# Optimization experiments

Measured on AMD Instinct MI355X. Metric: run time of the kernel, lower is better.

The kernel has to match this reference:

```python
import jax, jax.numpy as jnp
import numpy as np

N_NODES = 50000; N_EDGES = 600000; N_GRAPHS = 128
IN_CH = 128; PROJ = 128; OUT_CH = 128; K = 3; NCLASS = 2; EPS = 1e-5


def _mask():
    # xhi_layer_mask: block i (rows i*OUT_CH:(i+1)*OUT_CH) sees first PROJ*(i+1) input cols
    blocks = []
    for i in range(K):
        m = np.zeros((OUT_CH, PROJ * K), np.float32)
        m[:, :PROJ * (i + 1)] = 1.0
        blocks.append(m)
    return jnp.asarray(np.concatenate(blocks, 0))


def _bn(x, g, b):
    # BatchNorm1d in training mode: biased batch stats, affine g/b
    m = jnp.mean(x, axis=0)
    v = jnp.var(x, axis=0)
    return (x - m) * jax.lax.rsqrt(v + EPS) * g + b


def setup_inputs() -> dict:
    key = jax.random.key(0)
    ks = jax.random.split(key, 10)
    M = OUT_CH * K
    def w(k, shape):
        return jax.random.normal(k, shape, jnp.float32) * 0.05
    return {
        "x": jax.random.normal(ks[0], (N_NODES, IN_CH), jnp.float32),
        "edge_index": jax.random.randint(ks[1], (2, N_EDGES), 0, N_NODES),
        "batch": jnp.sort(jax.random.randint(ks[2], (N_NODES,), 0, N_GRAPHS)),
        "n_graphs": N_GRAPHS,
        "w_rel": w(ks[3], (PROJ, IN_CH)), "b_rel": jnp.zeros((PROJ,), jnp.float32),
        "w_root": w(ks[4], (PROJ, IN_CH)),
        "norm0_g": jnp.ones((PROJ,), jnp.float32), "norm0_b": jnp.zeros((PROJ,), jnp.float32),
        "lin_w": w(ks[5], (M, PROJ * K)), "lin_b": jnp.zeros((M,), jnp.float32),
        "bnh_g": jnp.ones((M,), jnp.float32), "bnh_b": jnp.zeros((M,), jnp.float32),
        "bno_g": jnp.ones((3 * M,), jnp.float32), "bno_b": jnp.zeros((3 * M,), jnp.float32),
        "w1": w(ks[6], (2 * M, 3 * M)), "b1": jnp.zeros((2 * M,), jnp.float32),
        "w2": w(ks[7], (M, 2 * M)), "b2": jnp.zeros((M,), jnp.float32),
        "w3": w(ks[8], (NCLASS, M)), "b3": jnp.zeros((NCLASS,), jnp.float32),
    }


def reference(x, edge_index, batch, n_graphs, w_rel, b_rel, w_root, norm0_g, norm0_b,
              lin_w, lin_b, bnh_g, bnh_b, bno_g, bno_b, w1, b1, w2, b2, w3, b3):
    row, col = edge_index[0], edge_index[1]
    # GraphConv: lin_rel(sum_{j->i} x_j) + lin_root(x_i)
    neigh = jax.ops.segment_sum(x[row], col, num_segments=N_NODES)
    X = neigh @ w_rel.T + b_rel + x @ w_root.T
    X = _bn(X, norm0_g, norm0_b)
    # k-hop polynomial diffusion: A^i X computed as iterative SpMM over edges
    # (A[r,c] = 1 for edge (r,c): (A v)[r] = sum over edges of v[c])
    H = [X]
    cur = X
    for _ in range(K - 1):
        cur = jax.ops.segment_sum(cur[col], row, num_segments=N_NODES)
        H.append(cur)
    Hc = jnp.concatenate(H, axis=1)  # [N, PROJ*K]
    Hm = _bn(Hc @ (lin_w * _mask()).T + lin_b, bnh_g, bnh_b)  # [N, OUT_CH*K]
    # global mean / add / max pooling per graph
    ones = jnp.ones((N_NODES,), jnp.float32)
    cnt = jax.ops.segment_sum(ones, batch, num_segments=n_graphs)
    Hadd = jax.ops.segment_sum(Hm, batch, num_segments=n_graphs)
    Havg = Hadd / jnp.maximum(cnt, 1.0)[:, None]
    Hmax = jax.ops.segment_max(Hm, batch, num_segments=n_graphs)
    Hmax = jnp.where(jnp.isfinite(Hmax), Hmax, 0.0)  # guard empty segments
    Hcat = jnp.concatenate([Havg, Hadd, Hmax], axis=1)  # [G, 3*OUT_CH*K]
    # funnel readout (dropout = identity in eval)
    h = _bn(Hcat, bno_g, bno_b)
    h = jax.nn.relu(h @ w1.T + b1)
    h = jax.nn.relu(h @ w2.T + b2)
    return jax.nn.log_softmax(h @ w3.T + b3, axis=1)
```

## Files before the change

kernel.cpp:

```cpp
#include <hip/hip_runtime.h>
#include <math.h>

#define N_NODES 50000
#define N_EDGES 600000
#define N_GRAPHS 128
#define IN_CH 128
#define PROJ 128
#define OUT_CH 128
#define M_DIM 384
#define HC_DIM 384
#define CAT_DIM 1152
#define H1_DIM 768
#define EPS 1e-5f
#define SCAN_BLK 256

using bf16x8 = __attribute__((ext_vector_type(8))) short;
using f32x4  = __attribute__((ext_vector_type(4))) float;

__device__ inline unsigned short f2bf(float f) {
  unsigned u = __float_as_uint(f);
  unsigned r = u + 0x7fffu + ((u >> 16) & 1u);
  return (unsigned short)(r >> 16);
}
__device__ inline float bf2f(unsigned short h) {
  return __uint_as_float(((unsigned)h) << 16);
}

__device__ inline void atomicMaxF(float* addr, float val) {
  int iv = __float_as_int(val);
  if (iv >= 0) atomicMax((int*)addr, iv);
  else         atomicMin((unsigned int*)addr, (unsigned int)iv);
}
__device__ inline void atomicMinF(float* addr, float val) {
  int iv = __float_as_int(val);
  if (iv >= 0) atomicMin((int*)addr, iv);
  else         atomicMax((unsigned int*)addr, (unsigned int)iv);
}

__global__ void fill_minmax_kernel(float* __restrict__ gmax, float* __restrict__ gmin) {
  int i = blockIdx.x * blockDim.x + threadIdx.x;
  if (i < N_GRAPHS * M_DIM) {
    gmax[i] = -__builtin_inff();
    gmin[i] =  __builtin_inff();
  }
}

__global__ void bounds_kernel(const int* __restrict__ batch, int* __restrict__ start) {
  int i = blockIdx.x * blockDim.x + threadIdx.x;
  if (i >= N_NODES) return;
  int b = batch[i];
  int bp = (i == 0) ? -1 : batch[i - 1];
  for (int g = bp + 1; g <= b; ++g) start[g] = i;
  if (i == N_NODES - 1)
    for (int g = b + 1; g <= N_GRAPHS; ++g) start[g] = N_NODES;
}

__global__ void cnt_from_bounds_kernel(const int* __restrict__ start, float* __restrict__ cnt) {
  int g = threadIdx.x;
  if (g < N_GRAPHS) cnt[g] = (float)(start[g + 1] - start[g]);
}

__global__ void hist_kernel(const int* __restrict__ row, const int* __restrict__ col,
                            int* __restrict__ degA, int* __restrict__ degB) {
  int e = blockIdx.x * blockDim.x + threadIdx.x;
  if (e < N_EDGES) {
    atomicAdd(&degA[col[e]], 1);
    atomicAdd(&degB[row[e]], 1);
  }
}

__global__ void scan1_kernel(const int* __restrict__ deg, int* __restrict__ offs,
                             int* __restrict__ bsum, int n) {
  __shared__ int sh[SCAN_BLK];
  int i = blockIdx.x * SCAN_BLK + threadIdx.x;
  int v = (i < n) ? deg[i] : 0;
  sh[threadIdx.x] = v; __syncthreads();
  #pragma unroll
  for (int d = 1; d < SCAN_BLK; d <<= 1) {
    int t = (threadIdx.x >= d) ? sh[threadIdx.x - d] : 0;
    __syncthreads();
    sh[threadIdx.x] += t;
    __syncthreads();
  }
  if (i < n) offs[i] = sh[threadIdx.x] - v;
  if (threadIdx.x == SCAN_BLK - 1) bsum[blockIdx.x] = sh[threadIdx.x];
}

__global__ void scan2_kernel(int* __restrict__ bsum, int nb) {
  __shared__ int sh[SCAN_BLK];
  int v = (threadIdx.x < nb) ? bsum[threadIdx.x] : 0;
  sh[threadIdx.x] = v; __syncthreads();
  #pragma unroll
  for (int d = 1; d < SCAN_BLK; d <<= 1) {
    int t = (threadIdx.x >= d) ? sh[threadIdx.x - d] : 0;
    __syncthreads();
    sh[threadIdx.x] += t;
    __syncthreads();
  }
  if (threadIdx.x < nb) bsum[threadIdx.x] = sh[threadIdx.x] - v;
}

__global__ void scan3_kernel(int* __restrict__ offs, const int* __restrict__ bsum,
                             int* __restrict__ cursor, int n) {
  int i = blockIdx.x * SCAN_BLK + threadIdx.x;
  if (i < n) {
    int o = offs[i] + bsum[blockIdx.x];
    offs[i] = o;
    cursor[i] = o;
  }
}

__global__ void fill_csr_kernel(const int* __restrict__ row, const int* __restrict__ col,
                                int* __restrict__ cursA, int* __restrict__ eidxA,
                                int* __restrict__ cursB, int* __restrict__ eidxB) {
  int e = blockIdx.x * blockDim.x + threadIdx.x;
  if (e < N_EDGES) {
    int r = row[e], c = col[e];
    eidxA[atomicAdd(&cursA[c], 1)] = r;
    eidxB[atomicAdd(&cursB[r], 1)] = c;
  }
}

__global__ void convert_x_kernel(const float* __restrict__ x, unsigned short* __restrict__ xnb) {
  int t = blockIdx.x * blockDim.x + threadIdx.x;
  if (t >= N_NODES * 32) return;
  int node = t >> 5;
  int c4 = (t & 31) << 2;
  float4 v = *(const float4*)(x + (size_t)node * IN_CH + c4);
  ushort4 h = {f2bf(v.x), f2bf(v.y), f2bf(v.z), f2bf(v.w)};
  *(ushort4*)(xnb + (size_t)node * 256 + 128 + c4) = h;
}

__global__ void convert_wcat_kernel(const float* __restrict__ w_rel, const float* __restrict__ w_root,
                                    unsigned short* __restrict__ wcatb) {
  int t = blockIdx.x * blockDim.x + threadIdx.x;
  if (t >= 128 * 64) return;
  int n = t >> 6;
  int c4 = (t & 63) << 2;
  const float* src = (c4 < 128) ? (w_rel + (size_t)n * 128 + c4)
                                : (w_root + (size_t)n * 128 + (c4 - 128));
  float4 v = *(const float4*)src;
  ushort4 h = {f2bf(v.x), f2bf(v.y), f2bf(v.z), f2bf(v.w)};
  *(ushort4*)(wcatb + (size_t)n * 256 + c4) = h;
}

__global__ void convert_linw_kernel(const float* __restrict__ lin_w, unsigned short* __restrict__ linwb) {
  int t = blockIdx.x * blockDim.x + threadIdx.x;
  if (t >= 384 * 96) return;
  int n = t / 96;
  int c4 = (t - n * 96) << 2;
  float4 v = *(const float4*)(lin_w + (size_t)n * HC_DIM + c4);
  ushort4 h = {f2bf(v.x), f2bf(v.y), f2bf(v.z), f2bf(v.w)};
  *(ushort4*)(linwb + (size_t)n * HC_DIM + c4) = h;
}

__global__ __launch_bounds__(256) void gather_bf16_kernel(
    const unsigned short* __restrict__ src, const int* __restrict__ offs,
    const int* __restrict__ ends, const int* __restrict__ eidx,
    unsigned short* __restrict__ dst, int src_ld, int dst_ld) {
  int tid = blockIdx.x * blockDim.x + threadIdx.x;
  int node = tid >> 5;
  int c = (tid & 31) << 2;
  if (node >= N_NODES) return;
  int j = offs[node], end = ends[node];
  float ax = 0.f, ay = 0.f, az = 0.f, aw = 0.f;
  for (; j + 1 < end; j += 2) {
    int s0 = eidx[j], s1 = eidx[j + 1];
    ushort4 v0 = *(const ushort4*)(src + (size_t)s0 * src_ld + c);
    ushort4 v1 = *(const ushort4*)(src + (size_t)s1 * src_ld + c);
    ax += bf2f(v0.x); ay += bf2f(v0.y); az += bf2f(v0.z); aw += bf2f(v0.w);
    ax += bf2f(v1.x); ay += bf2f(v1.y); az += bf2f(v1.z); aw += bf2f(v1.w);
  }
  if (j < end) {
    int s0 = eidx[j];
    ushort4 v0 = *(const ushort4*)(src + (size_t)s0 * src_ld + c);
    ax += bf2f(v0.x); ay += bf2f(v0.y); az += bf2f(v0.z); aw += bf2f(v0.w);
  }
  ushort4 h = {f2bf(ax), f2bf(ay), f2bf(az), f2bf(aw)};
  *(ushort4*)(dst + (size_t)node * dst_ld + c) = h;
}

__device__ inline void stage_tile(const unsigned short* __restrict__ src, int src_ld,
                                  int row0, int k0, int max_rows,
                                  char* __restrict__ zone, int t) {
  int r = t >> 1;
  int half = t & 1;
  const char* p = (const char*)(src + (size_t)(row0 + r) * src_ld + k0) + half * 64;
  bool ok = (row0 + r) < max_rows;
  #pragma unroll
  for (int jj = 0; jj < 4; ++jj) {
    uint4 v = make_uint4(0u, 0u, 0u, 0u);
    if (ok) v = *(const uint4*)(p + jj * 16);
    int slot = half * 4 + jj;
    *(uint4*)(zone + r * 128 + ((slot ^ (r & 7)) << 4)) = v;
  }
}

__device__ inline bf16x8 frag_ld(const char* __restrict__ zone, int row, int slot) {
  return *(const bf16x8*)(zone + row * 128 + ((slot ^ (row & 7)) << 4));
}

__global__ __launch_bounds__(256) void gemm_conv_mfma(
    const unsigned short* __restrict__ xnb, const unsigned short* __restrict__ wcatb,
    const float* __restrict__ b_rel, float* __restrict__ Hc0) {
  __shared__ char smem[32768];
  char* zoneA = smem;
  char* zoneB = smem + 16384;
  const int bm = blockIdx.x * 128;
  const int t = threadIdx.x;
  const int l = t & 63;
  const int wid = t >> 6;
  const int wr = wid >> 1, wc = wid & 1;
  const int lrow = l & 15, lk = l >> 4;
  f32x4 acc[4][4];
  #pragma unroll
  for (int i = 0; i < 4; ++i)
    #pragma unroll
    for (int jn = 0; jn < 4; ++jn) acc[i][jn] = (f32x4){0.f, 0.f, 0.f, 0.f};
  for (int st = 0; st < 4; ++st) {
    __syncthreads();
    stage_tile(xnb, 256, bm, st * 64, N_NODES, zoneA, t);
    stage_tile(wcatb, 256, 0, st * 64, 1 << 30, zoneB, t);
    __syncthreads();
    #pragma unroll
    for (int kk = 0; kk < 2; ++kk) {
      bf16x8 af[4], bfr[4];
      #pragma unroll
      for (int mf = 0; mf < 4; ++mf) af[mf] = frag_ld(zoneA, wr * 64 + mf * 16 + lrow, kk * 4 + lk);
      #pragma unroll
      for (int nf = 0; nf < 4; ++nf) bfr[nf] = frag_ld(zoneB, wc * 64 + nf * 16 + lrow, kk * 4 + lk);
      #pragma unroll
      for (int mf = 0; mf < 4; ++mf)
        #pragma unroll
        for (int nf = 0; nf < 4; ++nf)
          acc[mf][nf] = __builtin_amdgcn_mfma_f32_16x16x32_bf16(af[mf], bfr[nf], acc[mf][nf], 0, 0, 0);
    }
  }
  float brv[4];
  #pragma unroll
  for (int nf = 0; nf < 4; ++nf) brv[nf] = b_rel[wc * 64 + nf * 16 + lrow];
  #pragma unroll
  for (int mf = 0; mf < 4; ++mf) {
    #pragma unroll
    for (int q = 0; q < 4; ++q) {
      int r = bm + wr * 64 + mf * 16 + lk * 4 + q;
      if (r < N_NODES) {
        #pragma unroll
        for (int nf = 0; nf < 4; ++nf)
          Hc0[(size_t)r * 128 + wc * 64 + nf * 16 + lrow] = acc[mf][nf][q] + brv[nf];
      }
    }
  }
}

__global__ __launch_bounds__(256) void gemm_mask_mfma(
    const unsigned short* __restrict__ Hcb, const unsigned short* __restrict__ linwb,
    const float* __restrict__ lin_b, const int* __restrict__ batch,
    float* __restrict__ gsum, float* __restrict__ gmax, float* __restrict__ gmin,
    float* __restrict__ colsumsq) {
  __shared__ char smem[33792];
  __shared__ int bsh[128];
  char* zoneA = smem;
  char* zoneB = smem + 16384;
  const int bm = blockIdx.x * 128;
  const int bn = blockIdx.y * 128;
  const int nstages = 2 * (blockIdx.y + 1);
  const int t = threadIdx.x;
  const int l = t & 63;
  const int wid = t >> 6;
  const int wr = wid >> 1, wc = wid & 1;
  const int lrow = l & 15, lk = l >> 4;
  f32x4 acc[4][4];
  #pragma unroll
  for (int i = 0; i < 4; ++i)
    #pragma unroll
    for (int jn = 0; jn < 4; ++jn) acc[i][jn] = (f32x4){0.f, 0.f, 0.f, 0.f};
  for (int st = 0; st < nstages; ++st) {
    __syncthreads();
    stage_tile(Hcb, HC_DIM, bm, st * 64, N_NODES, zoneA, t);
    stage_tile(linwb, HC_DIM, bn, st * 64, 1 << 30, zoneB, t);
    __syncthreads();
    #pragma unroll
    for (int kk = 0; kk < 2; ++kk) {
      bf16x8 af[4], bfr[4];
      #pragma unroll
      for (int mf = 0; mf < 4; ++mf) af[mf] = frag_ld(zoneA, wr * 64 + mf * 16 + lrow, kk * 4 + lk);
      #pragma unroll
      for (int nf = 0; nf < 4; ++nf) bfr[nf] = frag_ld(zoneB, wc * 64 + nf * 16 + lrow, kk * 4 + lk);
      #pragma unroll
      for (int mf = 0; mf < 4; ++mf)
        #pragma unroll
        for (int nf = 0; nf < 4; ++nf)
          acc[mf][nf] = __builtin_amdgcn_mfma_f32_16x16x32_bf16(af[mf], bfr[nf], acc[mf][nf], 0, 0, 0);
    }
  }
  float lbv[4];
  #pragma unroll
  for (int nf = 0; nf < 4; ++nf) lbv[nf] = lin_b[bn + wc * 64 + nf * 16 + lrow];
  if (t < 128) bsh[t] = (bm + t < N_NODES) ? batch[bm + t] : -1;
  float* Y = (float*)smem;
  const int col = t & 127;
  const int gcol = bn + col;
  const int r0 = (t >> 7) * 32;
  float sq = 0.f;
  __syncthreads();
  for (int half = 0; half < 2; ++half) {
    if (wr == half) {
      #pragma unroll
      for (int mf = 0; mf < 4; ++mf)
        #pragma unroll
        for (int q = 0; q < 4; ++q) {
          int rr = mf * 16 + lk * 4 + q;
          #pragma unroll
          for (int nf = 0; nf < 4; ++nf)
            Y[rr * 132 + wc * 64 + nf * 16 + lrow] = acc[mf][nf][q] + lbv[nf];
        }
    }
    __syncthreads();
    int curg = -1;
    float s = 0.f, mx = 0.f, mn = 0.f;
    for (int rr = 0; rr < 32; ++rr) {
      int g = bsh[half * 64 + r0 + rr];
      if (g < 0) break;
      float y = Y[(r0 + rr) * 132 + col];
      sq += y * y;
      if (g != curg) {
        if (curg >= 0) {
          atomicAdd(&gsum[curg * M_DIM + gcol], s);
          atomicMaxF(&gmax[curg * M_DIM + gcol], mx);
          atomicMinF(&gmin[curg * M_DIM + gcol], mn);
        }
        curg = g; s = y; mx = y; mn = y;
      } else {
        s += y; mx = fmaxf(mx, y); mn = fminf(mn, y);
      }
    }
    if (curg >= 0) {
      atomicAdd(&gsum[curg * M_DIM + gcol], s);
      atomicMaxF(&gmax[curg * M_DIM + gcol], mx);
      atomicMinF(&gmin[curg * M_DIM + gcol], mn);
    }
    __syncthreads();
  }
  atomicAdd(&colsumsq[gcol], sq);
}

__global__ __launch_bounds__(256) void colstats0_kernel(
    const float* __restrict__ Hc0, float* __restrict__ colsum0, float* __restrict__ colsumsq0) {
  __shared__ float sh[256];
  int c = threadIdx.x & 127;
  int h = threadIdx.x >> 7;
  int r0 = blockIdx.x * 256;
  int rend = min(r0 + 256, N_NODES);
  float s = 0.f, q = 0.f;
  for (int r = r0 + h; r < rend; r += 2) {
    float v = Hc0[(size_t)r * 128 + c];
    s += v; q += v * v;
  }
  sh[threadIdx.x] = s; __syncthreads();
  if (h == 0) atomicAdd(&colsum0[c], sh[c] + sh[c + 128]);
  __syncthreads();
  sh[threadIdx.x] = q; __syncthreads();
  if (h == 0) atomicAdd(&colsumsq0[c], sh[c] + sh[c + 128]);
}

__global__ __launch_bounds__(256) void bn_apply0_kernel(
    const float* __restrict__ Hc0, unsigned short* __restrict__ Hcb,
    const float* __restrict__ colsum0, const float* __restrict__ colsumsq0,
    const float* __restrict__ g_, const float* __restrict__ b_) {
  int tid = blockIdx.x * blockDim.x + threadIdx.x;
  if (tid >= N_NODES * 32) return;
  int r = tid >> 5;
  int c = (tid & 31) << 2;
  float4 v = *(const float4*)(Hc0 + (size_t)r * 128 + c);
  float vv[4] = {v.x, v.y, v.z, v.w};
  #pragma unroll
  for (int j = 0; j < 4; ++j) {
    float m = colsum0[c + j] * (1.0f / N_NODES);
    float var = colsumsq0[c + j] * (1.0f / N_NODES) - m * m;
    float s = g_[c + j] * rsqrtf(var + EPS);
    float tt = b_[c + j] - m * s;
    vv[j] = vv[j] * s + tt;
  }
  ushort4 hh = {f2bf(vv[0]), f2bf(vv[1]), f2bf(vv[2]), f2bf(vv[3])};
  *(ushort4*)(Hcb + (size_t)r * HC_DIM + c) = hh;
}

__device__ inline float block_sum128(float v, float* red) {
  int t = threadIdx.x;
  red[t] = v; __syncthreads();
  #pragma unroll
  for (int s = 64; s >= 1; s >>= 1) {
    if (t < s) red[t] += red[t + s];
    __syncthreads();
  }
  float r = red[0];
  __syncthreads();
  return r;
}

__device__ inline void bn_write_col(float v, int col, const float* __restrict__ bg,
                                    const float* __restrict__ bb, float* __restrict__ h0T,
                                    float* red) {
  float s1 = block_sum128(v, red);
  float s2 = block_sum128(v * v, red);
  float m = s1 * (1.0f / N_GRAPHS);
  float var = s2 * (1.0f / N_GRAPHS) - m * m;
  float sc = bg[col] * rsqrtf(var + EPS);
  h0T[(size_t)col * N_GRAPHS + threadIdx.x] = (v - m) * sc + bb[col];
}

__global__ __launch_bounds__(128) void finalize_kernel(
    const float* __restrict__ gsum, const float* __restrict__ gmax,
    const float* __restrict__ gmin, const float* __restrict__ colsumsq,
    const float* __restrict__ cnt, const float* __restrict__ bnh_g,
    const float* __restrict__ bnh_b, const float* __restrict__ bno_g,
    const float* __restrict__ bno_b, float* __restrict__ h0T) {
  __shared__ float red[128];
  int c = blockIdx.x;
  int g = threadIdx.x;
  float vsum = gsum[g * M_DIM + c];
  float colsum = block_sum128(vsum, red);
  float m = colsum * (1.0f / N_NODES);
  float var = colsumsq[c] * (1.0f / N_NODES) - m * m;
  float s = bnh_g[c] * rsqrtf(var + EPS);
  float t = bnh_b[c] - m * s;
  float cg = cnt[g];
  float hadd = s * vsum + cg * t;
  float havg = hadd / fmaxf(cg, 1.0f);
  float hmax = 0.f;
  if (cg > 0.f)
    hmax = (s >= 0.f ? s * gmax[g * M_DIM + c] : s * gmin[g * M_DIM + c]) + t;
  bn_write_col(havg, c,        bno_g, bno_b, h0T, red);
  bn_write_col(hadd, 384 + c,  bno_g, bno_b, h0T, red);
  bn_write_col(hmax, 768 + c,  bno_g, bno_b, h0T, red);
}

__global__ __launch_bounds__(128) void mlp_kernel(
    const float* __restrict__ inT, const float* __restrict__ W,
    const float* __restrict__ bias, float* __restrict__ outT, int Kdim, int do_relu) {
  __shared__ float wrow[CAT_DIM];
  int oc = blockIdx.x;
  int g = threadIdx.x;
  for (int k = g; k < Kdim; k += 128) wrow[k] = W[(size_t)oc * Kdim + k];
  __syncthreads();
  float acc = bias[oc];
  for (int k = 0; k < Kdim; ++k) acc += inT[(size_t)k * N_GRAPHS + g] * wrow[k];
  if (do_relu) acc = fmaxf(acc, 0.f);
  outT[(size_t)oc * N_GRAPHS + g] = acc;
}

__global__ __launch_bounds__(128) void head_kernel(
    const float* __restrict__ h2T, const float* __restrict__ w3,
    const float* __restrict__ b3, float* __restrict__ out) {
  int g = threadIdx.x;
  float z0 = b3[0], z1 = b3[1];
  for (int k = 0; k < M_DIM; ++k) {
    float v = h2T[(size_t)k * N_GRAPHS + g];
    z0 += v * w3[k];
    z1 += v * w3[M_DIM + k];
  }
  float mz = fmaxf(z0, z1);
  float lse = mz + logf(expf(z0 - mz) + expf(z1 - mz));
  out[g * 2 + 0] = z0 - lse;
  out[g * 2 + 1] = z1 - lse;
}

extern "C" void kernel_launch(void* const* d_in, const int* in_sizes, int n_in,
                              void* d_out, int out_size, void* d_ws, size_t ws_size,
                              hipStream_t stream) {
  const float* x       = (const float*)d_in[0];
  const int*   row     = (const int*)d_in[1];
  const int*   col     = row + N_EDGES;
  const int*   batch   = (const int*)d_in[2];
  const float* w_rel   = (const float*)d_in[4];
  const float* b_rel   = (const float*)d_in[5];
  const float* w_root  = (const float*)d_in[6];
  const float* norm0_g = (const float*)d_in[7];
  const float* norm0_b = (const float*)d_in[8];
  const float* lin_w   = (const float*)d_in[9];
  const float* lin_b   = (const float*)d_in[10];
  const float* bnh_g   = (const float*)d_in[11];
  const float* bnh_b   = (const float*)d_in[12];
  const float* bno_g   = (const float*)d_in[13];
  const float* bno_b   = (const float*)d_in[14];
  const float* w1      = (const float*)d_in[15];
  const float* b1      = (const float*)d_in[16];
  const float* w2      = (const float*)d_in[17];
  const float* b2      = (const float*)d_in[18];
  const float* w3      = (const float*)d_in[19];
  const float* b3      = (const float*)d_in[20];
  float* out = (float*)d_out;

  char* ws = (char*)d_ws;
  size_t off = 0;
  auto allocb = [&](size_t nbytes) {
    char* p = ws + off;
    off += ((nbytes + 255) & ~(size_t)255);
    return p;
  };
  int*   degA      = (int*)allocb(N_NODES * 4);
  int*   degB      = (int*)allocb(N_NODES * 4);
  float* gsum      = (float*)allocb((size_t)N_GRAPHS * M_DIM * 4);
  float* colsumsq  = (float*)allocb(M_DIM * 4);
  float* colsum0   = (float*)allocb(PROJ * 4);
  float* colsumsq0 = (float*)allocb(PROJ * 4);
  size_t zero_bytes = off;
  float* cnt   = (float*)allocb(N_GRAPHS * 4);
  int*   gstart = (int*)allocb((N_GRAPHS + 1) * 4);
  int*   offsA = (int*)allocb(N_NODES * 4);
  int*   cursA = (int*)allocb(N_NODES * 4);
  int*   offsB = (int*)allocb(N_NODES * 4);
  int*   cursB = (int*)allocb(N_NODES * 4);
  int*   bsumA = (int*)allocb(SCAN_BLK * 4);
  int*   bsumB = (int*)allocb(SCAN_BLK * 4);
  int*   eidxA = (int*)allocb(N_EDGES * 4);
  int*   eidxB = (int*)allocb(N_EDGES * 4);
  float* Hc0   = (float*)allocb((size_t)N_NODES * 128 * 4);
  unsigned short* Hcb   = (unsigned short*)allocb((size_t)N_NODES * HC_DIM * 2);
  unsigned short* xnb   = (unsigned short*)allocb((size_t)N_NODES * 256 * 2);
  unsigned short* wcatb = (unsigned short*)allocb(128 * 256 * 2);
  unsigned short* linwb = (unsigned short*)allocb(384 * 384 * 2);
  float* gmax  = (float*)allocb((size_t)N_GRAPHS * M_DIM * 4);
  float* gmin  = (float*)allocb((size_t)N_GRAPHS * M_DIM * 4);
  float* h0T   = (float*)allocb((size_t)CAT_DIM * N_GRAPHS * 4);
  float* h1T   = (float*)allocb((size_t)H1_DIM * N_GRAPHS * 4);
  float* h2T   = (float*)allocb((size_t)M_DIM * N_GRAPHS * 4);

  const int NB = (N_NODES + SCAN_BLK - 1) / SCAN_BLK;

  hipMemsetAsync(d_ws, 0, zero_bytes, stream);
  fill_minmax_kernel<<<(N_GRAPHS * M_DIM + 255) / 256, 256, 0, stream>>>(gmax, gmin);
  bounds_kernel<<<(N_NODES + 255) / 256, 256, 0, stream>>>(batch, gstart);
  cnt_from_bounds_kernel<<<1, 128, 0, stream>>>(gstart, cnt);

  hist_kernel<<<(N_EDGES + 255) / 256, 256, 0, stream>>>(row, col, degA, degB);
  scan1_kernel<<<NB, SCAN_BLK, 0, stream>>>(degA, offsA, bsumA, N_NODES);
  scan1_kernel<<<NB, SCAN_BLK, 0, stream>>>(degB, offsB, bsumB, N_NODES);
  scan2_kernel<<<1, SCAN_BLK, 0, stream>>>(bsumA, NB);
  scan2_kernel<<<1, SCAN_BLK, 0, stream>>>(bsumB, NB);
  scan3_kernel<<<NB, SCAN_BLK, 0, stream>>>(offsA, bsumA, cursA, N_NODES);
  scan3_kernel<<<NB, SCAN_BLK, 0, stream>>>(offsB, bsumB, cursB, N_NODES);
  fill_csr_kernel<<<(N_EDGES + 255) / 256, 256, 0, stream>>>(row, col, cursA, eidxA, cursB, eidxB);

  convert_x_kernel<<<(N_NODES * 32 + 255) / 256, 256, 0, stream>>>(x, xnb);
  convert_wcat_kernel<<<(128 * 64 + 255) / 256, 256, 0, stream>>>(w_rel, w_root, wcatb);
  convert_linw_kernel<<<(384 * 96 + 255) / 256, 256, 0, stream>>>(lin_w, linwb);

  gather_bf16_kernel<<<(N_NODES * 32 + 255) / 256, 256, 0, stream>>>(
      xnb + 128, offsA, cursA, eidxA, xnb, 256, 256);
  gemm_conv_mfma<<<dim3((N_NODES + 127) / 128, 1), 256, 0, stream>>>(xnb, wcatb, b_rel, Hc0);
  colstats0_kernel<<<(N_NODES + 255) / 256, 256, 0, stream>>>(Hc0, colsum0, colsumsq0);
  bn_apply0_kernel<<<(N_NODES * 32 + 255) / 256, 256, 0, stream>>>(Hc0, Hcb, colsum0, colsumsq0, norm0_g, norm0_b);
  gather_bf16_kernel<<<(N_NODES * 32 + 255) / 256, 256, 0, stream>>>(
      Hcb, offsB, cursB, eidxB, Hcb + 128, HC_DIM, HC_DIM);
  gather_bf16_kernel<<<(N_NODES * 32 + 255) / 256, 256, 0, stream>>>(
      Hcb + 128, offsB, cursB, eidxB, Hcb + 256, HC_DIM, HC_DIM);
  gemm_mask_mfma<<<dim3((N_NODES + 127) / 128, 3), 256, 0, stream>>>(
      Hcb, linwb, lin_b, batch, gsum, gmax, gmin, colsumsq);
  finalize_kernel<<<M_DIM, 128, 0, stream>>>(gsum, gmax, gmin, colsumsq, cnt,
                                             bnh_g, bnh_b, bno_g, bno_b, h0T);
  mlp_kernel<<<H1_DIM, 128, 0, stream>>>(h0T, w1, b1, h1T, CAT_DIM, 1);
  mlp_kernel<<<M_DIM, 128, 0, stream>>>(h1T, w2, b2, h2T, H1_DIM, 1);
  head_kernel<<<1, 128, 0, stream>>>(h2T, w3, b3, out);
}
```

Before: 484.0 us.

## Partition CSR histogram and fill atomics by node range per block group

```diff
diff --git a/kernel.cpp b/kernel.cpp
--- a/kernel.cpp
+++ b/kernel.cpp
@@ -13,6 +13,9 @@
 #define H1_DIM 768
 #define EPS 1e-5f
 #define SCAN_BLK 256
+#define NPART 8
+#define PART_NODES 6250
+#define NPB 64
 
 using bf16x8 = __attribute__((ext_vector_type(8))) short;
 using f32x4  = __attribute__((ext_vector_type(4))) float;
@@ -60,12 +63,30 @@
   if (g < N_GRAPHS) cnt[g] = (float)(start[g + 1] - start[g]);
 }
 
-__global__ void hist_kernel(const int* __restrict__ row, const int* __restrict__ col,
-                            int* __restrict__ degA, int* __restrict__ degB) {
-  int e = blockIdx.x * blockDim.x + threadIdx.x;
-  if (e < N_EDGES) {
-    atomicAdd(&degA[col[e]], 1);
-    atomicAdd(&degB[row[e]], 1);
+__global__ __launch_bounds__(256) void hist_part_kernel(
+    const int* __restrict__ row, const int* __restrict__ col,
+    int* __restrict__ degA, int* __restrict__ degB) {
+  const int part = blockIdx.x & (NPART - 1);
+  const int slice = blockIdx.x >> 3;
+  const int lo = part * PART_NODES, hi = lo + PART_NODES;
+  for (int e = slice * 256 + threadIdx.x; e < N_EDGES; e += NPB * 256) {
+    int r = row[e], c = col[e];
+    if (c >= lo && c < hi) atomicAdd(&degA[c], 1);
+    if (r >= lo && r < hi) atomicAdd(&degB[r], 1);
+  }
+}
+
+__global__ __launch_bounds__(256) void fill_csr_part_kernel(
+    const int* __restrict__ row, const int* __restrict__ col,
+    int* __restrict__ cursA, int* __restrict__ eidxA,
+    int* __restrict__ cursB, int* __restrict__ eidxB) {
+  const int part = blockIdx.x & (NPART - 1);
+  const int slice = blockIdx.x >> 3;
+  const int lo = part * PART_NODES, hi = lo + PART_NODES;
+  for (int e = slice * 256 + threadIdx.x; e < N_EDGES; e += NPB * 256) {
+    int r = row[e], c = col[e];
+    if (c >= lo && c < hi) eidxA[atomicAdd(&cursA[c], 1)] = r;
+    if (r >= lo && r < hi) eidxB[atomicAdd(&cursB[r], 1)] = c;
   }
 }
 
@@ -107,17 +128,6 @@
     int o = offs[i] + bsum[blockIdx.x];
     offs[i] = o;
     cursor[i] = o;
-  }
-}
-
-__global__ void fill_csr_kernel(const int* __restrict__ row, const int* __restrict__ col,
-                                int* __restrict__ cursA, int* __restrict__ eidxA,
-                                int* __restrict__ cursB, int* __restrict__ eidxB) {
-  int e = blockIdx.x * blockDim.x + threadIdx.x;
-  if (e < N_EDGES) {
-    int r = row[e], c = col[e];
-    eidxA[atomicAdd(&cursA[c], 1)] = r;
-    eidxB[atomicAdd(&cursB[r], 1)] = c;
   }
 }
 
@@ -534,14 +544,14 @@
   bounds_kernel<<<(N_NODES + 255) / 256, 256, 0, stream>>>(batch, gstart);
   cnt_from_bounds_kernel<<<1, 128, 0, stream>>>(gstart, cnt);
 
-  hist_kernel<<<(N_EDGES + 255) / 256, 256, 0, stream>>>(row, col, degA, degB);
+  hist_part_kernel<<<NPART * NPB, 256, 0, stream>>>(row, col, degA, degB);
   scan1_kernel<<<NB, SCAN_BLK, 0, stream>>>(degA, offsA, bsumA, N_NODES);
   scan1_kernel<<<NB, SCAN_BLK, 0, stream>>>(degB, offsB, bsumB, N_NODES);
   scan2_kernel<<<1, SCAN_BLK, 0, stream>>>(bsumA, NB);
   scan2_kernel<<<1, SCAN_BLK, 0, stream>>>(bsumB, NB);
   scan3_kernel<<<NB, SCAN_BLK, 0, stream>>>(offsA, bsumA, cursA, N_NODES);
   scan3_kernel<<<NB, SCAN_BLK, 0, stream>>>(offsB, bsumB, cursB, N_NODES);
-  fill_csr_kernel<<<(N_EDGES + 255) / 256, 256, 0, stream>>>(row, col, cursA, eidxA, cursB, eidxB);
+  fill_csr_part_kernel<<<NPART * NPB, 256, 0, stream>>>(row, col, cursA, eidxA, cursB, eidxB);
 
   convert_x_kernel<<<(N_NODES * 32 + 255) / 256, 256, 0, stream>>>(x, xnb);
   convert_wcat_kernel<<<(128 * 64 + 255) / 256, 256, 0, stream>>>(w_rel, w_root, wcatb);
```

Measured after the change: 455.7 us. -5.9%, faster.
